# Optimization experiments

Hardware: AMD Instinct MI355X
Metric: run time of the kernel (lower is better)

Reference implementation:

```python
import jax, jax.numpy as jnp
import numpy as np

S, B, D, H = 2048, 2, 1024, 16
DK = D // H


def setup_inputs() -> dict:
    key = jax.random.key(0)
    k1, k2, k3 = jax.random.split(key, 3)
    x = jax.random.normal(k1, (S, B, D), dtype=jnp.float32)
    # xavier-uniform-like scale for weights
    w_qkv = jax.random.normal(k2, (3 * D, D), dtype=jnp.float32) * (1.0 / np.sqrt(D))
    w_out = jax.random.normal(k3, (D, D), dtype=jnp.float32) * (1.0 / np.sqrt(D))
    b_out = jnp.zeros((D,), dtype=jnp.float32)
    return {"x": x, "w_qkv": w_qkv, "w_out": w_out, "b_out": b_out}


def reference(x, w_qkv, w_out, b_out):
    seq_len, batch, d_model = x.shape
    n_heads = H
    d_k = d_model // n_heads
    # qkv projection: [S,B,3D]
    qkv = jnp.einsum('sbd,ed->sbe', x, w_qkv)
    qkv = qkv.reshape(seq_len, batch, 3, n_heads, d_k)
    qkv = jnp.transpose(qkv, (2, 1, 3, 0, 4))  # [3,B,H,S,dk]
    q, k, v = qkv[0], qkv[1], qkv[2]
    scores = jnp.einsum('bhqd,bhkd->bhqk', q, k) / jnp.sqrt(jnp.asarray(d_k, x.dtype))
    causal = jnp.triu(jnp.ones((seq_len, seq_len), dtype=bool), k=1)
    scores = jnp.where(causal[None, None], jnp.asarray(-jnp.inf, scores.dtype), scores)
    weights = jax.nn.softmax(scores, axis=-1)
    out = jnp.einsum('bhqk,bhkd->bhqd', weights, v)  # [B,H,S,dk]
    out = jnp.transpose(out, (2, 0, 1, 3)).reshape(seq_len, batch, d_model)
    return jnp.einsum('sbd,ed->sbe', out, w_out) + b_out
```

## Files before the change

### kernel.cpp

```cpp
#include <hip/hip_runtime.h>
#include <cstdint>

typedef _Float16 f16;
typedef _Float16 f16x4 __attribute__((ext_vector_type(4)));
typedef _Float16 f16x8 __attribute__((ext_vector_type(8)));
typedef float f32x4 __attribute__((ext_vector_type(4)));

#define MFMA16(a, b, c) __builtin_amdgcn_mfma_f32_16x16x32_f16(a, b, c, 0, 0, 0)
#define QSCALE 0.1803368801111243f

__device__ __forceinline__ void gload_lds16(const void* g, void* l) {
    __builtin_amdgcn_global_load_lds((__attribute__((address_space(1))) void*)(g),
                                     (__attribute__((address_space(3))) void*)(l),
                                     16, 0, 0);
}


__global__ void cast_all(const float* __restrict__ x, const float* __restrict__ wqv,
                         const float* __restrict__ wo, f16* __restrict__ out) {
    int i = blockIdx.x * blockDim.x + threadIdx.x;
    const float* src; int li;
    if (i < 1048576)      { src = x;   li = i; }
    else if (i < 1835008) { src = wqv; li = i - 1048576; }
    else                  { src = wo;  li = i - 1835008; }
    float4 v = reinterpret_cast<const float4*>(src)[li];
    f16x4 o = {(f16)v.x, (f16)v.y, (f16)v.z, (f16)v.w};
    reinterpret_cast<f16x4*>(out)[i] = o;
}

__global__ __launch_bounds__(256, 3) void gemm_qkv(
    const f16* __restrict__ A, const f16* __restrict__ B,
    f16* __restrict__ outq, f16* __restrict__ outk, f16* __restrict__ outvt)
{
    __shared__ f16 As[3][128 * 32];
    __shared__ f16 Bs[3][128 * 32];
    const int tid = threadIdx.x;
    const int lane = tid & 63;
    const int wave = tid >> 6;
    const int wm = wave >> 1, wn = wave & 1;

    const int wlin = blockIdx.x + 24 * blockIdx.y;
    const int xcd = wlin & 7;
    const int ii = wlin >> 3;
    const int bxx = 12 * (xcd & 1) + (ii % 12);
    const int byy = 8 * (xcd >> 1) + (ii / 12);

    const int bm = byy * 128, bn = bxx * 128;
    const int fr = lane & 15, fq = lane >> 4;

    const int srow = tid >> 2;
    const int su = (tid & 3) ^ (srow & 3) ^ ((srow >> 2) & 3);
    const int uoff = (fq ^ (fr & 3) ^ ((fr >> 2) & 3)) * 8;

    f32x4 acc[4][4] = {};

    auto stg = [&](int tt, int buf) {
        const int k0 = tt * 32;
        gload_lds16(&A[(bm + srow) * 1024 + k0 + su * 8],      &As[buf][tid * 8]);
        gload_lds16(&A[(bm + 64 + srow) * 1024 + k0 + su * 8], &As[buf][2048 + tid * 8]);
        gload_lds16(&B[(bn + srow) * 1024 + k0 + su * 8],      &Bs[buf][tid * 8]);
        gload_lds16(&B[(bn + 64 + srow) * 1024 + k0 + su * 8], &Bs[buf][2048 + tid * 8]);
    };

    auto step = [&](int t, int buf) {
        const int b2 = (buf + 2 >= 3) ? (buf - 1) : (buf + 2);
        if (t < 30) stg(t + 2, b2);
        f16x8 af[4], bf[4];
#pragma unroll
        for (int mt = 0; mt < 4; ++mt)
            af[mt] = *(const f16x8*)&As[buf][(wm * 64 + mt * 16 + fr) * 32 + uoff];
#pragma unroll
        for (int nt = 0; nt < 4; ++nt)
            bf[nt] = *(const f16x8*)&Bs[buf][(wn * 64 + nt * 16 + fr) * 32 + uoff];
        __builtin_amdgcn_s_setprio(1);
#pragma unroll
        for (int mt = 0; mt < 4; ++mt)
#pragma unroll
            for (int nt = 0; nt < 4; ++nt)
                acc[mt][nt] = MFMA16(af[mt], bf[nt], acc[mt][nt]);
        __builtin_amdgcn_s_setprio(0);
        if (t < 30) { asm volatile("s_waitcnt vmcnt(4)" ::: "memory"); }
        else        { asm volatile("s_waitcnt vmcnt(0)" ::: "memory"); }
        __builtin_amdgcn_s_barrier();
        __builtin_amdgcn_sched_barrier(0);
    };

    stg(0, 0);
    stg(1, 1);
    asm volatile("s_waitcnt vmcnt(4)" ::: "memory");
    __builtin_amdgcn_s_barrier();
    __builtin_amdgcn_sched_barrier(0);
#pragma unroll 1
    for (int tb = 0; tb < 30; tb += 3) {
        step(tb, 0);
        step(tb + 1, 1);
        step(tb + 2, 2);
    }
    step(30, 0);
    step(31, 1);

    const int x = bxx;
    if (x < 16) {
        f16* base = (x < 8) ? outq : outk;
        const float scale = (x < 8) ? QSCALE : 1.0f;
        const int coloff = (x < 8) ? bn : (bn - 1024);
#pragma unroll
        for (int mt = 0; mt < 4; ++mt)
#pragma unroll
            for (int nt = 0; nt < 4; ++nt)
#pragma unroll
                for (int i = 0; i < 4; ++i) {
                    int row = bm + wm * 64 + mt * 16 + fq * 4 + i;
                    int col = coloff + wn * 64 + nt * 16 + fr;
                    int s = row >> 1, b = row & 1;
                    int h = col >> 6, dk = col & 63;
                    base[((b * 16 + h) * 2048 + s) * 64 + dk] = (f16)(acc[mt][nt][i] * scale);
                }
    } else {
        const int xb = x - 16;
        const int s0 = bm >> 1;
        f16* Ts = &As[0][0];
#pragma unroll
        for (int p = 0; p < 2; ++p) {
            __syncthreads();
            if (wn == p) {
#pragma unroll
                for (int mt = 0; mt < 4; ++mt)
#pragma unroll
                    for (int nt = 0; nt < 4; ++nt)
#pragma unroll
                        for (int i = 0; i < 4; ++i) {
                            int row = wm * 64 + mt * 16 + fq * 4 + i;
                            int cl = nt * 16 + fr;
                            Ts[(cl * 2 + (row & 1)) * 76 + (row >> 1)] = (f16)acc[mt][nt][i];
                        }
            }
            __syncthreads();
            const int h = xb * 2 + p;
            const int sj = tid & 7;
#pragma unroll
            for (int it = 0; it < 4; ++it) {
                int idx = (tid >> 3) + it * 32;
                int bsel = idx & 1, dk = idx >> 1;
                f16x8 v = *(const f16x8*)&Ts[(dk * 2 + bsel) * 76 + sj * 8];
                *(f16x8*)&outvt[((bsel * 16 + h) * 64 + dk) * 2048 + s0 + sj * 8] = v;
            }
        }
    }
}

__global__ __launch_bounds__(512) void attn_kernel(
    const f16* __restrict__ qg, const f16* __restrict__ kg,
    const f16* __restrict__ vtg, f16* __restrict__ attn)
{
    __shared__ f16 Ks[2][2 * 4096];
    __shared__ f16 Vs[2][2 * 4096];
    __shared__ f16 plds[8][16 * 64];
    const int tid = threadIdx.x;
    const int lane = tid & 63;
    const int wave = tid >> 6;

    const int w = blockIdx.x + (blockIdx.y << 4);
    const int xcd = w & 7;
    const int idx = w >> 3;
    const int bh = xcd + ((idx & 3) << 3);
    const int qpair = idx >> 2;

    const int b = bh >> 4, h = bh & 15;
    const int fr = lane & 15, fq = lane >> 4;

    const bool isB = wave < 4;
    const int w4 = wave & 3;
    const int qrow = (isB ? (31 - qpair) : qpair) * 64 + w4 * 16;
    const int nB = 32 - qpair;
    const int nK = isB ? nB : (qpair + 1);

    const f16* Q  = qg  + bh * 2048 * 64;
    const f16* K  = kg  + bh * 2048 * 64;
    const f16* VT = vtg + bh * 64 * 2048;
    f16* P = plds[wave];
    const int pswz = (fr & 7) << 3;

    const int sr = tid >> 3;
    const int scu = (tid & 7) ^ (sr & 7);

    f16x8 aq0 = *(const f16x8*)&Q[(qrow + fr) * 64 + fq * 8];
    f16x8 aq1 = *(const f16x8*)&Q[(qrow + fr) * 64 + 32 + fq * 8];

    f32x4 o[4] = {};
    float lsum = 0.f;

    auto stage64 = [&](int kc, int buf, int hh) {
        const int kb = kc * 64;
        gload_lds16(&K[(kb + sr) * 64 + scu * 8], &Ks[buf][hh * 4096 + tid * 8]);
        gload_lds16(&VT[sr * 2048 + kb + scu * 8], &Vs[buf][hh * 4096 + tid * 8]);
    };

    auto compute = [&](int kb, const f16* Ksb, const f16* Vsb, bool domask) {
        f32x4 sc[4] = {};
        __builtin_amdgcn_s_setprio(1);
#pragma unroll
        for (int ct = 0; ct < 4; ++ct) {
            int r = ct * 16 + fr;
            f16x8 kf0 = *(const f16x8*)&Ksb[r * 64 + ((fq ^ (r & 7)) * 8)];
            f16x8 kf1 = *(const f16x8*)&Ksb[r * 64 + (((4 + fq) ^ (r & 7)) * 8)];
            sc[ct] = MFMA16(kf0, aq0, sc[ct]);
            sc[ct] = MFMA16(kf1, aq1, sc[ct]);
        }
        __builtin_amdgcn_s_setprio(0);
        if (domask) {
#pragma unroll
            for (int ct = 0; ct < 4; ++ct) {
                int kk = kb + ct * 16 + fq * 4;
#pragma unroll
                for (int i = 0; i < 4; ++i)
                    if (kk + i > qrow + fr) sc[ct][i] = -1e30f;
            }
        }
#pragma unroll
        for (int ct = 0; ct < 4; ++ct) {
            float p0 = __builtin_amdgcn_exp2f(sc[ct][0]);
            float p1 = __builtin_amdgcn_exp2f(sc[ct][1]);
            float p2 = __builtin_amdgcn_exp2f(sc[ct][2]);
            float p3 = __builtin_amdgcn_exp2f(sc[ct][3]);
            lsum += (p0 + p1) + (p2 + p3);
            f16x4 pk = {(f16)p0, (f16)p1, (f16)p2, (f16)p3};
            *(f16x4*)&P[fr * 64 + ((ct * 16 + fq * 4) ^ pswz)] = pk;
        }
        f16x8 ap0 = *(const f16x8*)&P[fr * 64 + ((fq * 8) ^ pswz)];
        f16x8 ap1 = *(const f16x8*)&P[fr * 64 + ((32 + fq * 8) ^ pswz)];
        __builtin_amdgcn_s_setprio(1);
#pragma unroll
        for (int nt = 0; nt < 4; ++nt) {
            int dk = nt * 16 + fr;
            f16x8 bv0 = *(const f16x8*)&Vsb[dk * 64 + ((fq ^ (dk & 7)) * 8)];
            f16x8 bv1 = *(const f16x8*)&Vsb[dk * 64 + (((4 + fq) ^ (dk & 7)) * 8)];
            o[nt] = MFMA16(ap0, bv0, o[nt]);
            o[nt] = MFMA16(ap1, bv1, o[nt]);
        }
        __builtin_amdgcn_s_setprio(0);
    };

    stage64(0, 0, 0);
    stage64(1, 0, 1);
    asm volatile("s_waitcnt vmcnt(0)" ::: "memory");
    __builtin_amdgcn_s_barrier();
    __builtin_amdgcn_sched_barrier(0);

    const int nP = (nB + 1) >> 1;
#pragma unroll 1
    for (int ip = 0; ip < nP; ++ip) {
        const int buf = ip & 1;
        if (ip + 1 < nP) {
            stage64(2 * ip + 2, buf ^ 1, 0);
            if (2 * ip + 3 < nB) stage64(2 * ip + 3, buf ^ 1, 1);
        }
        const int kc0 = 2 * ip, kc1 = 2 * ip + 1;
        if (kc0 < nK) compute(kc0 * 64, &Ks[buf][0],    &Vs[buf][0],    kc0 * 64 + 63 > qrow);
        if (kc1 < nK) compute(kc1 * 64, &Ks[buf][4096], &Vs[buf][4096], kc1 * 64 + 63 > qrow);
        asm volatile("s_waitcnt vmcnt(0)" ::: "memory");
        __builtin_amdgcn_s_barrier();
        __builtin_amdgcn_sched_barrier(0);
    }

    float rs = lsum;
    rs += __shfl_xor(rs, 16);
    rs += __shfl_xor(rs, 32);
    float inv = __builtin_amdgcn_rcpf(rs);
#pragma unroll
    for (int i = 0; i < 4; ++i) {
        float invi = __shfl(inv, fq * 4 + i);
        int srow = qrow + fq * 4 + i;
#pragma unroll
        for (int nt = 0; nt < 4; ++nt)
            attn[(srow * 2 + b) * 1024 + h * 64 + nt * 16 + fr] = (f16)(o[nt][i] * invi);
    }
}

__global__ __launch_bounds__(256) void gemm_out(
    const f16* __restrict__ A, const f16* __restrict__ B,
    const float* __restrict__ bias, float* __restrict__ out)
{
    __shared__ f16 As[3][128 * 32];
    __shared__ f16 Bs[3][64 * 32];
    const int tid = threadIdx.x;
    const int lane = tid & 63;
    const int wave = tid >> 6;
    const int wm = wave >> 1, wn = wave & 1;

    const int wlin = blockIdx.x + 16 * blockIdx.y;
    const int xcd = wlin & 7;
    const int ii = wlin >> 3;
    const int bxx = 8 * (xcd & 1) + (ii & 7);
    const int byy = 8 * (xcd >> 1) + (ii >> 3);

    const int bm = byy * 128, bn = bxx * 64;
    const int fr = lane & 15, fq = lane >> 4;

    const int srow = tid >> 2;
    const int su = (tid & 3) ^ (srow & 3) ^ ((srow >> 2) & 3);
    const int uoff = (fq ^ (fr & 3) ^ ((fr >> 2) & 3)) * 8;

    f32x4 acc[4][2] = {};

    auto stg = [&](int tt, int buf) {
        const int k0 = tt * 32;
        gload_lds16(&A[(bm + srow) * 1024 + k0 + su * 8],      &As[buf][tid * 8]);
        gload_lds16(&A[(bm + 64 + srow) * 1024 + k0 + su * 8], &As[buf][2048 + tid * 8]);
        gload_lds16(&B[(bn + srow) * 1024 + k0 + su * 8],      &Bs[buf][tid * 8]);
    };

    auto step = [&](int t, int buf) {
        const int b2 = (buf + 2 >= 3) ? (buf - 1) : (buf + 2);
        if (t < 30) stg(t + 2, b2);
        f16x8 af[4], bf[2];
#pragma unroll
        for (int mt = 0; mt < 4; ++mt)
            af[mt] = *(const f16x8*)&As[buf][(wm * 64 + mt * 16 + fr) * 32 + uoff];
#pragma unroll
        for (int nt = 0; nt < 2; ++nt)
            bf[nt] = *(const f16x8*)&Bs[buf][(wn * 32 + nt * 16 + fr) * 32 + uoff];
        __builtin_amdgcn_s_setprio(1);
#pragma unroll
        for (int mt = 0; mt < 4; ++mt)
#pragma unroll
            for (int nt = 0; nt < 2; ++nt)
                acc[mt][nt] = MFMA16(af[mt], bf[nt], acc[mt][nt]);
        __builtin_amdgcn_s_setprio(0);
        if (t < 30) { asm volatile("s_waitcnt vmcnt(3)" ::: "memory"); }
        else        { asm volatile("s_waitcnt vmcnt(0)" ::: "memory"); }
        __builtin_amdgcn_s_barrier();
        __builtin_amdgcn_sched_barrier(0);
    };

    stg(0, 0);
    stg(1, 1);
    asm volatile("s_waitcnt vmcnt(3)" ::: "memory");
    __builtin_amdgcn_s_barrier();
    __builtin_amdgcn_sched_barrier(0);
#pragma unroll 1
    for (int tb = 0; tb < 30; tb += 3) {
        step(tb, 0);
        step(tb + 1, 1);
        step(tb + 2, 2);
    }
    step(30, 0);
    step(31, 1);

#pragma unroll
    for (int mt = 0; mt < 4; ++mt)
#pragma unroll
        for (int nt = 0; nt < 2; ++nt)
#pragma unroll
            for (int i = 0; i < 4; ++i) {
                int row = bm + wm * 64 + mt * 16 + fq * 4 + i;
                int col = bn + wn * 32 + nt * 16 + fr;
                out[row * 1024 + col] = acc[mt][nt][i] + bias[col];
            }
}

extern "C" void kernel_launch(void* const* d_in, const int* in_sizes, int n_in,
                              void* d_out, int out_size, void* d_ws, size_t ws_size,
                              hipStream_t stream)
{
    const float* x     = (const float*)d_in[0];
    const float* w_qkv = (const float*)d_in[1];
    const float* w_out = (const float*)d_in[2];
    const float* b_out = (const float*)d_in[3];
    float* out = (float*)d_out;

    char* ws = (char*)d_ws;
    f16* xh  = (f16*)(ws);
    f16* wqh = (f16*)(ws + 8388608);
    f16* woh = (f16*)(ws + 14680064);
    f16* qh  = (f16*)(ws + 16777216);
    f16* kh  = (f16*)(ws + 25165824);
    f16* vt  = (f16*)(ws + 33554432);
    f16* ah  = (f16*)(ws + 41943040);

    cast_all<<<8192, 256, 0, stream>>>(x, w_qkv, w_out, xh);
    gemm_qkv<<<dim3(24, 32), 256, 0, stream>>>(xh, wqh, qh, kh, vt);
    attn_kernel<<<dim3(16, 32), 512, 0, stream>>>(qh, kh, vt, ah);
    gemm_out<<<dim3(16, 32), 256, 0, stream>>>(ah, woh, b_out, out);
}
```

Before: 165.2 us.

## Switch attention to 32x32 MFMA with in-register P via permlane32 swap

Rewrites the attention kernel to use 32x32x16 MFMA tiles, with each wave owning 32 query rows instead of 16. The probability matrix is repacked into MFMA operand layout in registers using v_permlane32_swap rather than a round trip through LDS. Blocks shrink from 512 to 256 threads with two blocks per CU, and staging issues four loads per thread. The change aims to cut LDS traffic and instruction count, at the cost of higher register pressure per wave and some dead leftover variables.

```diff
diff --git a/kernel.cpp b/kernel.cpp
--- a/kernel.cpp
+++ b/kernel.cpp
@@ -2,17 +2,25 @@
 #include <cstdint>
 
 typedef _Float16 f16;
+typedef _Float16 f16x2 __attribute__((ext_vector_type(2)));
 typedef _Float16 f16x4 __attribute__((ext_vector_type(4)));
 typedef _Float16 f16x8 __attribute__((ext_vector_type(8)));
 typedef float f32x4 __attribute__((ext_vector_type(4)));
+typedef float f32x16 __attribute__((ext_vector_type(16)));
 
 #define MFMA16(a, b, c) __builtin_amdgcn_mfma_f32_16x16x32_f16(a, b, c, 0, 0, 0)
+#define MFMA32(a, b, c) __builtin_amdgcn_mfma_f32_32x32x16_f16(a, b, c, 0, 0, 0)
 #define QSCALE 0.1803368801111243f
 
 __device__ __forceinline__ void gload_lds16(const void* g, void* l) {
     __builtin_amdgcn_global_load_lds((__attribute__((address_space(1))) void*)(g),
                                      (__attribute__((address_space(3))) void*)(l),
                                      16, 0, 0);
+}
+
+__device__ __forceinline__ unsigned pack2(float x, float y) {
+    f16x2 t = {(f16)x, (f16)y};
+    return __builtin_bit_cast(unsigned, t);
 }
 
 
@@ -149,16 +157,21 @@
     }
 }
 
-__global__ __launch_bounds__(512) void attn_kernel(
+__global__ __launch_bounds__(256, 2) void attn_kernel(
     const f16* __restrict__ qg, const f16* __restrict__ kg,
     const f16* __restrict__ vtg, f16* __restrict__ attn)
 {
-    __shared__ f16 Ks[2][2 * 4096];
-    __shared__ f16 Vs[2][2 * 4096];
-    __shared__ f16 plds[8][16 * 64];
+    __shared__ __align__(16) char smem[65536];
+    f16* KsB = (f16*)smem;
+    f16* VsB = (f16*)(smem + 32768);
+    float* comb   = (float*)smem;
+    float* comb_l = (float*)(smem + 32768);
+
     const int tid = threadIdx.x;
     const int lane = tid & 63;
     const int wave = tid >> 6;
+    const int l31 = lane & 31;
+    const int hi = lane >> 5;
 
     const int w = blockIdx.x + (blockIdx.y << 4);
     const int xcd = w & 7;
@@ -167,78 +180,86 @@
     const int qpair = idx >> 2;
 
     const int b = bh >> 4, h = bh & 15;
-    const int fr = lane & 15, fq = lane >> 4;
-
-    const bool isB = wave < 4;
-    const int w4 = wave & 3;
-    const int qrow = (isB ? (31 - qpair) : qpair) * 64 + w4 * 16;
+
+    const bool isB = wave < 2 || wave < 4 ? (wave < 4 && (wave >> 2) == 0) : false;
+    const int sub = wave & 1;
+    const int par = (wave >> 1) & 1;
+    const int tile = (wave < 2 || par == ((wave >> 1) & 1)) ? 0 : 0;
+    const int mytile = (wave < 2) ? (31 - qpair) : qpair;
+    const int qrow = mytile * 64 + sub * 32;
     const int nB = 32 - qpair;
-    const int nK = isB ? nB : (qpair + 1);
+    const int nK = mytile + 1;
 
     const f16* Q  = qg  + bh * 2048 * 64;
     const f16* K  = kg  + bh * 2048 * 64;
     const f16* VT = vtg + bh * 64 * 2048;
-    f16* P = plds[wave];
-    const int pswz = (fr & 7) << 3;
-
-    const int sr = tid >> 3;
-    const int scu = (tid & 7) ^ (sr & 7);
-
-    f16x8 aq0 = *(const f16x8*)&Q[(qrow + fr) * 64 + fq * 8];
-    f16x8 aq1 = *(const f16x8*)&Q[(qrow + fr) * 64 + 32 + fq * 8];
-
-    f32x4 o[4] = {};
+
+    const int sr2 = tid >> 3;
+    const int scu = (tid & 7) ^ (sr2 & 7);
+
+    f16x8 aq[4];
+#pragma unroll
+    for (int t = 0; t < 4; ++t)
+        aq[t] = *(const f16x8*)&Q[(qrow + l31) * 64 + t * 16 + hi * 8];
+
+    f32x16 o0 = {}, o1 = {};
     float lsum = 0.f;
+    const int qmax = qrow + l31;
 
     auto stage64 = [&](int kc, int buf, int hh) {
         const int kb = kc * 64;
-        gload_lds16(&K[(kb + sr) * 64 + scu * 8], &Ks[buf][hh * 4096 + tid * 8]);
-        gload_lds16(&VT[sr * 2048 + kb + scu * 8], &Vs[buf][hh * 4096 + tid * 8]);
-    };
-
-    auto compute = [&](int kb, const f16* Ksb, const f16* Vsb, bool domask) {
-        f32x4 sc[4] = {};
+        f16* kd = KsB + buf * 8192 + hh * 4096;
+        f16* vd = VsB + buf * 8192 + hh * 4096;
+        gload_lds16(&K[(kb + sr2) * 64 + scu * 8],          &kd[tid * 8]);
+        gload_lds16(&K[(kb + sr2 + 32) * 64 + scu * 8],     &kd[2048 + tid * 8]);
+        gload_lds16(&VT[sr2 * 2048 + kb + scu * 8],         &vd[tid * 8]);
+        gload_lds16(&VT[(sr2 + 32) * 2048 + kb + scu * 8],  &vd[2048 + tid * 8]);
+    };
+
+    auto compute32 = [&](int kb, const f16* Ksb, const f16* Vsb, bool domask) {
+        f32x16 sc0 = {}, sc1 = {};
         __builtin_amdgcn_s_setprio(1);
 #pragma unroll
-        for (int ct = 0; ct < 4; ++ct) {
-            int r = ct * 16 + fr;
-            f16x8 kf0 = *(const f16x8*)&Ksb[r * 64 + ((fq ^ (r & 7)) * 8)];
-            f16x8 kf1 = *(const f16x8*)&Ksb[r * 64 + (((4 + fq) ^ (r & 7)) * 8)];
-            sc[ct] = MFMA16(kf0, aq0, sc[ct]);
-            sc[ct] = MFMA16(kf1, aq1, sc[ct]);
+        for (int t = 0; t < 4; ++t) {
+            f16x8 kf0 = *(const f16x8*)&Ksb[l31 * 64 + (((2 * t + hi) ^ (l31 & 7)) * 8)];
+            f16x8 kf1 = *(const f16x8*)&Ksb[(32 + l31) * 64 + (((2 * t + hi) ^ (l31 & 7)) * 8)];
+            sc0 = MFMA32(kf0, aq[t], sc0);
+            sc1 = MFMA32(kf1, aq[t], sc1);
         }
         __builtin_amdgcn_s_setprio(0);
-        if (domask) {
-#pragma unroll
-            for (int ct = 0; ct < 4; ++ct) {
-                int kk = kb + ct * 16 + fq * 4;
-#pragma unroll
-                for (int i = 0; i < 4; ++i)
-                    if (kk + i > qrow + fr) sc[ct][i] = -1e30f;
+        float p0[16], p1[16];
+#pragma unroll
+        for (int r = 0; r < 16; ++r) {
+            const int kl = (r & 3) + 8 * (r >> 2) + 4 * hi;
+            float s0 = sc0[r], s1 = sc1[r];
+            if (domask) {
+                if (kb + kl > qmax)      s0 = -1e30f;
+                if (kb + 32 + kl > qmax) s1 = -1e30f;
             }
+            float e0 = __builtin_amdgcn_exp2f(s0);
+            float e1 = __builtin_amdgcn_exp2f(s1);
+            p0[r] = e0; p1[r] = e1;
+            lsum += e0 + e1;
         }
 #pragma unroll
-        for (int ct = 0; ct < 4; ++ct) {
-            float p0 = __builtin_amdgcn_exp2f(sc[ct][0]);
-            float p1 = __builtin_amdgcn_exp2f(sc[ct][1]);
-            float p2 = __builtin_amdgcn_exp2f(sc[ct][2]);
-            float p3 = __builtin_amdgcn_exp2f(sc[ct][3]);
-            lsum += (p0 + p1) + (p2 + p3);
-            f16x4 pk = {(f16)p0, (f16)p1, (f16)p2, (f16)p3};
-            *(f16x4*)&P[fr * 64 + ((ct * 16 + fq * 4) ^ pswz)] = pk;
+        for (int ks = 0; ks < 4; ++ks) {
+            const int rb = 8 * (ks & 1);
+            const float* pp = (ks < 2) ? p0 : p1;
+            unsigned a0 = pack2(pp[rb + 0], pp[rb + 1]);
+            unsigned a1 = pack2(pp[rb + 2], pp[rb + 3]);
+            unsigned b0 = pack2(pp[rb + 4], pp[rb + 5]);
+            unsigned b1 = pack2(pp[rb + 6], pp[rb + 7]);
+            asm("v_permlane32_swap_b32 %0, %1" : "+v"(a0), "+v"(b0));
+            asm("v_permlane32_swap_b32 %0, %1" : "+v"(a1), "+v"(b1));
+            uint4 W = {a0, a1, b0, b1};
+            f16x8 apk = __builtin_bit_cast(f16x8, W);
+            f16x8 vf0 = *(const f16x8*)&Vsb[l31 * 64 + (((2 * ks + hi) ^ (l31 & 7)) * 8)];
+            f16x8 vf1 = *(const f16x8*)&Vsb[(32 + l31) * 64 + (((2 * ks + hi) ^ (l31 & 7)) * 8)];
+            __builtin_amdgcn_s_setprio(1);
+            o0 = MFMA32(apk, vf0, o0);
+            o1 = MFMA32(apk, vf1, o1);
+            __builtin_amdgcn_s_setprio(0);
         }
-        f16x8 ap0 = *(const f16x8*)&P[fr * 64 + ((fq * 8) ^ pswz)];
-        f16x8 ap1 = *(const f16x8*)&P[fr * 64 + ((32 + fq * 8) ^ pswz)];
-        __builtin_amdgcn_s_setprio(1);
-#pragma unroll
-        for (int nt = 0; nt < 4; ++nt) {
-            int dk = nt * 16 + fr;
-            f16x8 bv0 = *(const f16x8*)&Vsb[dk * 64 + ((fq ^ (dk & 7)) * 8)];
-            f16x8 bv1 = *(const f16x8*)&Vsb[dk * 64 + (((4 + fq) ^ (dk & 7)) * 8)];
-            o[nt] = MFMA16(ap0, bv0, o[nt]);
-            o[nt] = MFMA16(ap1, bv1, o[nt]);
-        }
-        __builtin_amdgcn_s_setprio(0);
     };
 
     stage64(0, 0, 0);
@@ -256,25 +277,27 @@
             if (2 * ip + 3 < nB) stage64(2 * ip + 3, buf ^ 1, 1);
         }
         const int kc0 = 2 * ip, kc1 = 2 * ip + 1;
-        if (kc0 < nK) compute(kc0 * 64, &Ks[buf][0],    &Vs[buf][0],    kc0 * 64 + 63 > qrow);
-        if (kc1 < nK) compute(kc1 * 64, &Ks[buf][4096], &Vs[buf][4096], kc1 * 64 + 63 > qrow);
+        const f16* Kb = KsB + buf * 8192;
+        const f16* Vb = VsB + buf * 8192;
+        if (kc0 < nK) compute32(kc0 * 64, Kb, Vb, kc0 * 64 + 63 > qrow);
+        if (kc1 < nK) compute32(kc1 * 64, Kb + 4096, Vb + 4096, kc1 * 64 + 63 > qrow);
         asm volatile("s_waitcnt vmcnt(0)" ::: "memory");
         __builtin_amdgcn_s_barrier();
         __builtin_amdgcn_sched_barrier(0);
+        if (false) (void)0;
     }
 
-    float rs = lsum;
-    rs += __shfl_xor(rs, 16);
-    rs += __shfl_xor(rs, 32);
+    float rs = lsum + __shfl_xor(lsum, 32);
     float inv = __builtin_amdgcn_rcpf(rs);
 #pragma unroll
-    for (int i = 0; i < 4; ++i) {
-        float invi = __shfl(inv, fq * 4 + i);
-        int srow = qrow + fq * 4 + i;
-#pragma unroll
-        for (int nt = 0; nt < 4; ++nt)
-            attn[(srow * 2 + b) * 1024 + h * 64 + nt * 16 + fr] = (f16)(o[nt][i] * invi);
+    for (int r = 0; r < 16; ++r) {
+        const int rq = (r & 3) + 8 * (r >> 2) + 4 * hi;
+        float invr = __shfl(inv, rq);
+        const int srow = qrow + rq;
+        attn[(srow * 2 + b) * 1024 + h * 64 + l31]      = (f16)(o0[r] * invr);
+        attn[(srow * 2 + b) * 1024 + h * 64 + 32 + l31] = (f16)(o1[r] * invr);
     }
+    (void)comb; (void)comb_l;
 }
 
 __global__ __launch_bounds__(256) void gemm_out(
@@ -380,6 +403,6 @@
 
     cast_all<<<8192, 256, 0, stream>>>(x, w_qkv, w_out, xh);
     gemm_qkv<<<dim3(24, 32), 256, 0, stream>>>(xh, wqh, qh, kh, vt);
-    attn_kernel<<<dim3(16, 32), 512, 0, stream>>>(qh, kh, vt, ah);
+    attn_kernel<<<dim3(16, 32), 256, 0, stream>>>(qh, kh, vt, ah);
     gemm_out<<<dim3(16, 32), 256, 0, stream>>>(ah, woh, b_out, out);
 }
```

After: 170.9 us. 3.4% more time.
